# Performance work log

Hardware: AMD Instinct MI355X
Metric: run time of the kernel (lower is better)

Reference implementation:

```python
import jax, jax.numpy as jnp
import numpy as np

EPS = 1e-05

def setup_inputs() -> dict:
    key = jax.random.key(0)
    k1, = jax.random.split(key, 1)
    x = jax.random.normal(k1, (4, 4096, 2048), dtype=jnp.float32)
    g = jnp.ones((2048,), dtype=jnp.float32)
    return {"x": x, "g": g}

def reference(x, g):
    # RMSNorm: x / sqrt(mean(x^2, axis=-1) + eps) * g, computed in fp32
    dtype = x.dtype
    xf = x.astype(jnp.float32)
    ms = jnp.mean(xf * xf, axis=-1, keepdims=True)  # [B,S,1]
    out = xf * jax.lax.rsqrt(ms + EPS) * g
    return out.astype(dtype)
```

## Files before the change

kernel.cpp:

```cpp
#include <hip/hip_runtime.h>

#define ROW_LEN 2048
#define WAVES_PER_BLOCK 4
#define BLOCK (WAVES_PER_BLOCK * 64)
#define V4_PER_LANE (ROW_LEN / 4 / 64)
#define EPS 1e-5f

typedef float vf4 __attribute__((ext_vector_type(4)));

__global__ __launch_bounds__(BLOCK) void RMSNorm_56607668961691_kernel(
    const vf4* __restrict__ x,
    const vf4* __restrict__ g,
    vf4* __restrict__ out,
    int rows)
{
    const int wave = threadIdx.x >> 6;
    const int lane = threadIdx.x & 63;
    const int row  = blockIdx.x * WAVES_PER_BLOCK + wave;
    if (row >= rows) return;

    const vf4* __restrict__ xr   = x   + (size_t)row * (ROW_LEN / 4);
    vf4* __restrict__       outr = out + (size_t)row * (ROW_LEN / 4);

    vf4 v[V4_PER_LANE];
    #pragma unroll
    for (int k = 0; k < V4_PER_LANE; ++k)
        v[k] = xr[lane + k * 64];

    float ss = 0.0f;
    #pragma unroll
    for (int k = 0; k < V4_PER_LANE; ++k)
        ss += v[k].x * v[k].x + v[k].y * v[k].y + v[k].z * v[k].z + v[k].w * v[k].w;

    #pragma unroll
    for (int off = 32; off > 0; off >>= 1)
        ss += __shfl_xor(ss, off, 64);

    const float scale = rsqrtf(ss * (1.0f / (float)ROW_LEN) + EPS);

    #pragma unroll
    for (int k = 0; k < V4_PER_LANE; ++k) {
        vf4 gk = g[lane + k * 64];
        vf4 o;
        o.x = v[k].x * scale * gk.x;
        o.y = v[k].y * scale * gk.y;
        o.z = v[k].z * scale * gk.z;
        o.w = v[k].w * scale * gk.w;
        __builtin_nontemporal_store(o, &outr[lane + k * 64]);
    }
}

extern "C" void kernel_launch(void* const* d_in, const int* in_sizes, int n_in,
                              void* d_out, int out_size, void* d_ws, size_t ws_size,
                              hipStream_t stream) {
    const vf4* x = (const vf4*)d_in[0];
    const vf4* g = (const vf4*)d_in[1];
    vf4* out = (vf4*)d_out;

    const int rows = in_sizes[0] / ROW_LEN;
    const int grid = (rows + WAVES_PER_BLOCK - 1) / WAVES_PER_BLOCK;
    RMSNorm_56607668961691_kernel<<<grid, BLOCK, 0, stream>>>(x, g, out, rows);
}
```

Measured before the change: 231.9 us.

## Process multiple rows per wave with software-prefetched next row and cached gamma

Each wave now normalizes four consecutive rows, loading gamma once into registers and prefetching the next row's data while reducing and writing the current one. This aims to hide load latency and drop repeated gamma loads. It also replaces nontemporal stores with regular stores. The cost is fewer waves in flight and higher register use, and rows not divisible by four are not bounds-checked.

```diff
diff --git a/kernel.cpp b/kernel.cpp
--- a/kernel.cpp
+++ b/kernel.cpp
@@ -1,9 +1,10 @@
 #include <hip/hip_runtime.h>
 
 #define ROW_LEN 2048
+#define V4_PER_LANE (ROW_LEN / 4 / 64)
+#define ROWS_PER_WAVE 4
 #define WAVES_PER_BLOCK 4
 #define BLOCK (WAVES_PER_BLOCK * 64)
-#define V4_PER_LANE (ROW_LEN / 4 / 64)
 #define EPS 1e-5f
 
 typedef float vf4 __attribute__((ext_vector_type(4)));
@@ -16,37 +17,61 @@
 {
     const int wave = threadIdx.x >> 6;
     const int lane = threadIdx.x & 63;
-    const int row  = blockIdx.x * WAVES_PER_BLOCK + wave;
-    if (row >= rows) return;
+    const int gwave = blockIdx.x * WAVES_PER_BLOCK + wave;
+    const int row0 = gwave * ROWS_PER_WAVE;
+    if (row0 >= rows) return;
 
-    const vf4* __restrict__ xr   = x   + (size_t)row * (ROW_LEN / 4);
-    vf4* __restrict__       outr = out + (size_t)row * (ROW_LEN / 4);
-
-    vf4 v[V4_PER_LANE];
+    vf4 gr[V4_PER_LANE];
     #pragma unroll
     for (int k = 0; k < V4_PER_LANE; ++k)
-        v[k] = xr[lane + k * 64];
+        gr[k] = g[lane + k * 64];
 
-    float ss = 0.0f;
+    const vf4* __restrict__ xr   = x   + (size_t)row0 * (ROW_LEN / 4);
+    vf4* __restrict__       outr = out + (size_t)row0 * (ROW_LEN / 4);
+
+    vf4 cur[V4_PER_LANE];
     #pragma unroll
     for (int k = 0; k < V4_PER_LANE; ++k)
-        ss += v[k].x * v[k].x + v[k].y * v[k].y + v[k].z * v[k].z + v[k].w * v[k].w;
+        cur[k] = xr[lane + k * 64];
 
     #pragma unroll
-    for (int off = 32; off > 0; off >>= 1)
-        ss += __shfl_xor(ss, off, 64);
+    for (int i = 0; i < ROWS_PER_WAVE; ++i) {
+        vf4 nxt[V4_PER_LANE];
+        if (i + 1 < ROWS_PER_WAVE) {
+            const vf4* __restrict__ xn = xr + (size_t)(i + 1) * (ROW_LEN / 4);
+            #pragma unroll
+            for (int k = 0; k < V4_PER_LANE; ++k)
+                nxt[k] = xn[lane + k * 64];
+        }
 
-    const float scale = rsqrtf(ss * (1.0f / (float)ROW_LEN) + EPS);
+        float ss = 0.0f;
+        #pragma unroll
+        for (int k = 0; k < V4_PER_LANE; ++k)
+            ss += cur[k].x * cur[k].x + cur[k].y * cur[k].y
+                + cur[k].z * cur[k].z + cur[k].w * cur[k].w;
 
-    #pragma unroll
-    for (int k = 0; k < V4_PER_LANE; ++k) {
-        vf4 gk = g[lane + k * 64];
-        vf4 o;
-        o.x = v[k].x * scale * gk.x;
-        o.y = v[k].y * scale * gk.y;
-        o.z = v[k].z * scale * gk.z;
-        o.w = v[k].w * scale * gk.w;
-        __builtin_nontemporal_store(o, &outr[lane + k * 64]);
+        #pragma unroll
+        for (int off = 32; off > 0; off >>= 1)
+            ss += __shfl_xor(ss, off, 64);
+
+        const float scale = rsqrtf(ss * (1.0f / (float)ROW_LEN) + EPS);
+
+        vf4* __restrict__ outn = outr + (size_t)i * (ROW_LEN / 4);
+        #pragma unroll
+        for (int k = 0; k < V4_PER_LANE; ++k) {
+            vf4 o;
+            o.x = cur[k].x * scale * gr[k].x;
+            o.y = cur[k].y * scale * gr[k].y;
+            o.z = cur[k].z * scale * gr[k].z;
+            o.w = cur[k].w * scale * gr[k].w;
+            outn[lane + k * 64] = o;
+        }
+
+        if (i + 1 < ROWS_PER_WAVE) {
+            #pragma unroll
+            for (int k = 0; k < V4_PER_LANE; ++k)
+                cur[k] = nxt[k];
+        }
     }
 }
 
@@ -58,6 +83,7 @@
     vf4* out = (vf4*)d_out;
 
     const int rows = in_sizes[0] / ROW_LEN;
-    const int grid = (rows + WAVES_PER_BLOCK - 1) / WAVES_PER_BLOCK;
+    const int waves = (rows + ROWS_PER_WAVE - 1) / ROWS_PER_WAVE;
+    const int grid  = (waves + WAVES_PER_BLOCK - 1) / WAVES_PER_BLOCK;
     RMSNorm_56607668961691_kernel<<<grid, BLOCK, 0, stream>>>(x, g, out, rows);
 }
```

Result: no change. 232.9 us (+0.4%).
